# Performance work log

Hardware: AMD Instinct MI355X
Metric: run time of the kernel (lower is better)

## Reference

```python
import jax, jax.numpy as jnp
import numpy as np

N_QUBITS = 7
N_LAYERS = 4
DIM = 2 ** N_QUBITS  # 128
# PennyLane StronglyEntanglingLayers default ranges: (l % (n_wires-1)) + 1
RANGES = [(l % (N_QUBITS - 1)) + 1 for l in range(N_LAYERS)]  # [1,2,3,4]
BATCH = 262144


def rot_matrix(phi, theta, omega):
    """PennyLane Rot(phi, theta, omega) = RZ(omega) RY(theta) RZ(phi)."""
    c = jnp.cos(theta / 2)
    s = jnp.sin(theta / 2)
    a = jnp.exp(-0.5j * (phi + omega)) * c
    b = -jnp.exp(0.5j * (phi - omega)) * s
    cc = jnp.exp(-0.5j * (phi - omega)) * s
    d = jnp.exp(0.5j * (phi + omega)) * c
    return jnp.stack([jnp.stack([a, b]), jnp.stack([cc, d])])  # (2,2) complex64


def apply_1q(psi, U, wire):
    # psi: (batch, 2,2,2,2,2,2,2); apply 2x2 U on qubit axis 1+wire
    psi = jnp.moveaxis(psi, 1 + wire, -1)
    psi = psi @ U.T
    return jnp.moveaxis(psi, -1, 1 + wire)


def apply_cnot(psi, ctrl, tgt):
    psi = jnp.moveaxis(psi, (1 + ctrl, 1 + tgt), (-2, -1))
    # flip target amplitude pair where control == 1
    psi = jnp.concatenate([psi[..., 0:1, :], psi[..., 1:2, ::-1]], axis=-2)
    return jnp.moveaxis(psi, (-2, -1), (1 + ctrl, 1 + tgt))


def setup_inputs() -> dict:
    key = jax.random.key(0)
    k1, k2 = jax.random.split(key)
    x = jax.random.normal(k1, (BATCH, DIM), dtype=jnp.float32)
    weights = jax.random.normal(k2, (N_LAYERS, N_QUBITS, 3), dtype=jnp.float32)
    return {"x": x, "weights": weights}


def reference(x, weights):
    # AmplitudeEmbedding with normalize=True
    norm = jnp.linalg.norm(x, axis=-1, keepdims=True)
    psi = (x / norm).astype(jnp.complex64)
    psi = psi.reshape((-1,) + (2,) * N_QUBITS)

    # StronglyEntanglingLayers
    for l in range(N_LAYERS):
        for w in range(N_QUBITS):
            U = rot_matrix(weights[l, w, 0], weights[l, w, 1], weights[l, w, 2])
            psi = apply_1q(psi, U, w)
        r = RANGES[l]
        for w in range(N_QUBITS):
            psi = apply_cnot(psi, w, (w + r) % N_QUBITS)

    # expval(Z0 @ Z6): sign = (-1)^(b0 + b6)
    probs = (jnp.abs(psi) ** 2).reshape(-1, 2, DIM // 4, 2)  # (batch, q0, mid, q6)
    z = jnp.array([1.0, -1.0], dtype=jnp.float32)
    return jnp.einsum('a,namb,b->n', z, probs, z)
```

## Files before the change

kernel.cpp:

```cpp
#include <hip/hip_runtime.h>


#define N_QUBITS 7
#define DIM 128
#define N_LAYERS 4
#define BATCH 262144
#define GRID 512
#define ROWS 32
#define ITERS (BATCH / (GRID * ROWS))
#define DEPTH 4

typedef short short8 __attribute__((ext_vector_type(8)));
typedef float f32x4 __attribute__((ext_vector_type(4)));
typedef unsigned int u32;
typedef __attribute__((address_space(1))) const u32 g_u32;
typedef __attribute__((address_space(3))) u32 l_u32;

__device__ __forceinline__ unsigned short f2bf(float f) {
  unsigned u = __builtin_bit_cast(unsigned, f);
  u += 0x7fffu + ((u >> 16) & 1u);
  return (unsigned short)(u >> 16);
}

__device__ __forceinline__ unsigned pk2(float x, float y) {
  unsigned ux = __builtin_bit_cast(unsigned, x) + 0x8000u;
  unsigned uy = __builtin_bit_cast(unsigned, y) + 0x8000u;
  return __builtin_amdgcn_perm(uy, ux, 0x07060302u);
}

__device__ __forceinline__ short8 pack_bf16(float4 lo, float4 hi) {
  uint4 d;
  d.x = pk2(lo.x, lo.y);
  d.y = pk2(lo.z, lo.w);
  d.z = pk2(hi.x, hi.y);
  d.w = pk2(hi.z, hi.w);
  return __builtin_bit_cast(short8, d);
}

__global__ void sim_columns(const float* __restrict__ W,
                            float* __restrict__ Ur, float* __restrict__ Ui) {
  __shared__ float sr[DIM], si[DIM];
  const int c = blockIdx.x;
  const int t = threadIdx.x;

  sr[t] = (t == c) ? 1.f : 0.f;        si[t] = 0.f;
  sr[t + 64] = (t + 64 == c) ? 1.f : 0.f;  si[t + 64] = 0.f;
  __syncthreads();

  for (int l = 0; l < N_LAYERS; ++l) {
    for (int w = 0; w < N_QUBITS; ++w) {
      const float phi = W[(l * 7 + w) * 3 + 0];
      const float th  = W[(l * 7 + w) * 3 + 1];
      const float om  = W[(l * 7 + w) * 3 + 2];
      const float ch = __cosf(0.5f * th), sh = __sinf(0.5f * th);
      const float ap = 0.5f * (phi + om), am = 0.5f * (phi - om);
      const float cap = __cosf(ap), sap = __sinf(ap);
      const float cam = __cosf(am), sam = __sinf(am);
      const float ar =  cap * ch, ai = -sap * ch;
      const float br = -cam * sh, bi = -sam * sh;
      const float cr =  cam * sh, ci = -sam * sh;
      const float dr =  cap * ch, di =  sap * ch;

      const int m = 1 << (6 - w);
      const int i0 = ((t & ~(m - 1)) << 1) | (t & (m - 1));
      const int i1 = i0 | m;
      const float x0r = sr[i0], x0i = si[i0];
      const float x1r = sr[i1], x1i = si[i1];
      __syncthreads();
      sr[i0] = ar * x0r - ai * x0i + br * x1r - bi * x1i;
      si[i0] = ar * x0i + ai * x0r + br * x1i + bi * x1r;
      sr[i1] = cr * x0r - ci * x0i + dr * x1r - di * x1i;
      si[i1] = cr * x0i + ci * x0r + dr * x1i + di * x1r;
      __syncthreads();
    }
    const int r = (l % (N_QUBITS - 1)) + 1;
    for (int w = 0; w < N_QUBITS; ++w) {
      const int ctrl = w, tgt = (w + r) % N_QUBITS;
      const int cmask = 1 << (6 - ctrl), tmask = 1 << (6 - tgt);
      const int i0 = ((t & ~(tmask - 1)) << 1) | (t & (tmask - 1));
      const int i1 = i0 | tmask;
      const float a0r = sr[i0], a0i = si[i0];
      const float a1r = sr[i1], a1i = si[i1];
      __syncthreads();
      if (i0 & cmask) {
        sr[i0] = a1r; si[i0] = a1i;
        sr[i1] = a0r; si[i1] = a0i;
      }
      __syncthreads();
    }
  }
  Ur[(size_t)t * DIM + c]        = sr[t];
  Ui[(size_t)t * DIM + c]        = si[t];
  Ur[(size_t)(t + 64) * DIM + c] = sr[t + 64];
  Ui[(size_t)(t + 64) * DIM + c] = si[t + 64];
}

__global__ void build_A(const float* __restrict__ Ur, const float* __restrict__ Ui,
                        unsigned short* __restrict__ Ab) {
  const int i = blockIdx.x;
  const int j = threadIdx.x;
  float s = 0.f;
#pragma unroll 8
  for (int k = 0; k < DIM; ++k) {
    const float zk = (((k >> 6) ^ k) & 1) ? -1.f : 1.f;
    s += zk * (Ur[k * DIM + i] * Ur[k * DIM + j] + Ui[k * DIM + i] * Ui[k * DIM + j]);
  }
  Ab[i * DIM + j] = f2bf(s);
}

__device__ __forceinline__ void stage_half(const float* __restrict__ X, float* XsBuf,
                                           int tile, int wave, int lane) {
#pragma unroll
  for (int j = 0; j < 8; ++j) {
    const int s = 512 * wave + 64 * j + lane;
    const int row = s >> 5;
    const int c = (s & 31) ^ (row & 7);
    const float* gp = X + (size_t)tile * (ROWS * DIM) + row * DIM + c * 4;
    __builtin_amdgcn_global_load_lds((g_u32*)gp, (l_u32*)(XsBuf + s * 4), 16, 0, 0);
  }
}

__global__ __launch_bounds__(128, 1) void vqa_main(const float* __restrict__ X,
                                                   const unsigned short* __restrict__ Ab,
                                                   float* __restrict__ out) {
  __shared__ float Xs[DEPTH * ROWS * DIM];

  const int tid = threadIdx.x;
  const int lane = tid & 63;
  const int wave = tid >> 6;
  const int n16 = lane & 15;
  const int g = lane >> 4;
  const int R = 16 * wave + n16;
  const int rx = R & 7;

  short8 a_frag[4][8];
#pragma unroll
  for (int kt = 0; kt < 4; ++kt)
#pragma unroll
    for (int t = 0; t < 8; ++t)
      a_frag[kt][t] = *reinterpret_cast<const short8*>(
          Ab + (16 * t + n16) * DIM + 32 * kt + 8 * g);

#pragma unroll
  for (int p = 0; p < DEPTH - 1; ++p)
    stage_half(X, Xs + p * (ROWS * DIM), blockIdx.x + p * GRID, wave, lane);

#pragma unroll 1
  for (int it = 0; it < ITERS; ++it) {
    const int cur = it & (DEPTH - 1);

    if (it + DEPTH - 1 < ITERS)
      stage_half(X, Xs + ((it + DEPTH - 1) & (DEPTH - 1)) * (ROWS * DIM),
                 blockIdx.x + (it + DEPTH - 1) * GRID, wave, lane);

    const int rem = ITERS - 1 - it;
    if (rem >= DEPTH - 1)  asm volatile("s_waitcnt vmcnt(24)" ::: "memory");
    else if (rem == 2)     asm volatile("s_waitcnt vmcnt(16)" ::: "memory");
    else if (rem == 1)     asm volatile("s_waitcnt vmcnt(8)"  ::: "memory");
    else                   asm volatile("s_waitcnt vmcnt(0)"  ::: "memory");

    const int rb = cur * (ROWS * 32) + R * 32;

    short8 bfrag[4];
#pragma unroll
    for (int kt = 0; kt < 4; ++kt) {
      const int c0 = 8 * kt + 2 * g;
      const float4 lo = *reinterpret_cast<const float4*>(Xs + (rb + (c0 ^ rx)) * 4);
      const float4 hi = *reinterpret_cast<const float4*>(Xs + (rb + ((c0 + 1) ^ rx)) * 4);
      bfrag[kt] = pack_bf16(lo, hi);
    }

    f32x4 acc[8];
#pragma unroll
    for (int t = 0; t < 8; ++t) acc[t] = (f32x4){0.f, 0.f, 0.f, 0.f};
#pragma unroll
    for (int kt = 0; kt < 4; ++kt) {
#pragma unroll
      for (int t = 0; t < 8; ++t)
        acc[t] = __builtin_amdgcn_mfma_f32_16x16x32_bf16(a_frag[kt][t], bfrag[kt],
                                                         acc[t], 0, 0, 0);
    }

    float dot = 0.f, nrm = 0.f;
#pragma unroll
    for (int t = 0; t < 8; ++t) {
      const float4 xe = *reinterpret_cast<const float4*>(Xs + (rb + ((4 * t + g) ^ rx)) * 4);
      dot += xe.x * acc[t][0] + xe.y * acc[t][1] + xe.z * acc[t][2] + xe.w * acc[t][3];
      nrm += xe.x * xe.x + xe.y * xe.y + xe.z * xe.z + xe.w * xe.w;
    }
    dot += __shfl_xor(dot, 16, 64);
    dot += __shfl_xor(dot, 32, 64);
    nrm += __shfl_xor(nrm, 16, 64);
    nrm += __shfl_xor(nrm, 32, 64);
    if (g == 0) out[(blockIdx.x + it * GRID) * ROWS + R] = dot / nrm;
  }
}

extern "C" void kernel_launch(void* const* d_in, const int* in_sizes, int n_in,
                              void* d_out, int out_size, void* d_ws, size_t ws_size,
                              hipStream_t stream) {
  const float* X = (const float*)d_in[0];
  const float* W = (const float*)d_in[1];
  float* out = (float*)d_out;

  float* Ur = (float*)d_ws;
  float* Ui = Ur + DIM * DIM;
  unsigned short* Ab = (unsigned short*)(Ui + DIM * DIM);

  sim_columns<<<DIM, 64, 0, stream>>>(W, Ur, Ui);
  build_A<<<DIM, DIM, 0, stream>>>(Ur, Ui, Ab);
  vqa_main<<<GRID, 128, 0, stream>>>(X, Ab, out);
}
```

Measured before the change: 208.4 us.

## Fuse circuit simulation, A-matrix build and main GEMV into one persistent kernel

Merges the three launches into a single kernel that uses software grid barriers. The first 128 blocks simulate the unitary columns with wave shuffles in registers instead of LDS plus syncthreads, then build the bf16 observable matrix. All 512 blocks wait on a second barrier before the main streaming loop. The X prefetch is issued before the setup phase so the loads overlap it. This removes launch gaps and the serialized small-kernel latency, but it adds a memset, depends on every block being co-resident for the spin barriers, and the barrier spin costs some time of its own.

```diff
diff --git a/kernel.cpp b/kernel.cpp
--- a/kernel.cpp
+++ b/kernel.cpp
@@ -37,75 +37,16 @@
   return __builtin_bit_cast(short8, d);
 }
 
-__global__ void sim_columns(const float* __restrict__ W,
-                            float* __restrict__ Ur, float* __restrict__ Ui) {
-  __shared__ float sr[DIM], si[DIM];
-  const int c = blockIdx.x;
-  const int t = threadIdx.x;
-
-  sr[t] = (t == c) ? 1.f : 0.f;        si[t] = 0.f;
-  sr[t + 64] = (t + 64 == c) ? 1.f : 0.f;  si[t + 64] = 0.f;
+__device__ __forceinline__ void grid_bar(unsigned* bar, unsigned target) {
+  __threadfence();
   __syncthreads();
-
-  for (int l = 0; l < N_LAYERS; ++l) {
-    for (int w = 0; w < N_QUBITS; ++w) {
-      const float phi = W[(l * 7 + w) * 3 + 0];
-      const float th  = W[(l * 7 + w) * 3 + 1];
-      const float om  = W[(l * 7 + w) * 3 + 2];
-      const float ch = __cosf(0.5f * th), sh = __sinf(0.5f * th);
-      const float ap = 0.5f * (phi + om), am = 0.5f * (phi - om);
-      const float cap = __cosf(ap), sap = __sinf(ap);
-      const float cam = __cosf(am), sam = __sinf(am);
-      const float ar =  cap * ch, ai = -sap * ch;
-      const float br = -cam * sh, bi = -sam * sh;
-      const float cr =  cam * sh, ci = -sam * sh;
-      const float dr =  cap * ch, di =  sap * ch;
-
-      const int m = 1 << (6 - w);
-      const int i0 = ((t & ~(m - 1)) << 1) | (t & (m - 1));
-      const int i1 = i0 | m;
-      const float x0r = sr[i0], x0i = si[i0];
-      const float x1r = sr[i1], x1i = si[i1];
-      __syncthreads();
-      sr[i0] = ar * x0r - ai * x0i + br * x1r - bi * x1i;
-      si[i0] = ar * x0i + ai * x0r + br * x1i + bi * x1r;
-      sr[i1] = cr * x0r - ci * x0i + dr * x1r - di * x1i;
-      si[i1] = cr * x0i + ci * x0r + dr * x1i + di * x1r;
-      __syncthreads();
-    }
-    const int r = (l % (N_QUBITS - 1)) + 1;
-    for (int w = 0; w < N_QUBITS; ++w) {
-      const int ctrl = w, tgt = (w + r) % N_QUBITS;
-      const int cmask = 1 << (6 - ctrl), tmask = 1 << (6 - tgt);
-      const int i0 = ((t & ~(tmask - 1)) << 1) | (t & (tmask - 1));
-      const int i1 = i0 | tmask;
-      const float a0r = sr[i0], a0i = si[i0];
-      const float a1r = sr[i1], a1i = si[i1];
-      __syncthreads();
-      if (i0 & cmask) {
-        sr[i0] = a1r; si[i0] = a1i;
-        sr[i1] = a0r; si[i1] = a0i;
-      }
-      __syncthreads();
-    }
-  }
-  Ur[(size_t)t * DIM + c]        = sr[t];
-  Ui[(size_t)t * DIM + c]        = si[t];
-  Ur[(size_t)(t + 64) * DIM + c] = sr[t + 64];
-  Ui[(size_t)(t + 64) * DIM + c] = si[t + 64];
-}
-
-__global__ void build_A(const float* __restrict__ Ur, const float* __restrict__ Ui,
-                        unsigned short* __restrict__ Ab) {
-  const int i = blockIdx.x;
-  const int j = threadIdx.x;
-  float s = 0.f;
-#pragma unroll 8
-  for (int k = 0; k < DIM; ++k) {
-    const float zk = (((k >> 6) ^ k) & 1) ? -1.f : 1.f;
-    s += zk * (Ur[k * DIM + i] * Ur[k * DIM + j] + Ui[k * DIM + i] * Ui[k * DIM + j]);
-  }
-  Ab[i * DIM + j] = f2bf(s);
+  if (threadIdx.x == 0) {
+    __hip_atomic_fetch_add(bar, 1u, __ATOMIC_ACQ_REL, __HIP_MEMORY_SCOPE_AGENT);
+    while (__hip_atomic_load(bar, __ATOMIC_ACQUIRE, __HIP_MEMORY_SCOPE_AGENT) < target)
+      __builtin_amdgcn_s_sleep(8);
+    __threadfence();
+  }
+  __syncthreads();
 }
 
 __device__ __forceinline__ void stage_half(const float* __restrict__ X, float* XsBuf,
@@ -120,14 +61,111 @@
   }
 }
 
-__global__ __launch_bounds__(128, 1) void vqa_main(const float* __restrict__ X,
-                                                   const unsigned short* __restrict__ Ab,
-                                                   float* __restrict__ out) {
+__global__ __launch_bounds__(128, 1) void vqa_fused(const float* __restrict__ X,
+                                                    const float* __restrict__ W,
+                                                    float* __restrict__ Ur,
+                                                    float* __restrict__ Ui,
+                                                    unsigned short* __restrict__ Ab,
+                                                    unsigned* __restrict__ bars,
+                                                    float* __restrict__ out) {
   __shared__ float Xs[DEPTH * ROWS * DIM];
 
   const int tid = threadIdx.x;
   const int lane = tid & 63;
   const int wave = tid >> 6;
+
+#pragma unroll
+  for (int p = 0; p < DEPTH - 1; ++p)
+    stage_half(X, Xs + p * (ROWS * DIM), blockIdx.x + p * GRID, wave, lane);
+
+  if (blockIdx.x < DIM) {
+    if (wave == 0) {
+      const int c = blockIdx.x;
+      float r0r = (lane == c) ? 1.f : 0.f, r0i = 0.f;
+      float r1r = (lane + 64 == c) ? 1.f : 0.f, r1i = 0.f;
+
+      for (int l = 0; l < N_LAYERS; ++l) {
+        for (int w = 0; w < N_QUBITS; ++w) {
+          const float phi = W[(l * 7 + w) * 3 + 0];
+          const float th  = W[(l * 7 + w) * 3 + 1];
+          const float om  = W[(l * 7 + w) * 3 + 2];
+          const float ch = __cosf(0.5f * th), sh = __sinf(0.5f * th);
+          const float ap = 0.5f * (phi + om), am = 0.5f * (phi - om);
+          const float cap = __cosf(ap), sap = __sinf(ap);
+          const float cam = __cosf(am), sam = __sinf(am);
+          const float ar =  cap * ch, ai = -sap * ch;
+          const float br = -cam * sh, bi = -sam * sh;
+          const float cr =  cam * sh, ci = -sam * sh;
+          const float dr =  cap * ch, di =  sap * ch;
+
+          const int m = 1 << (6 - w);
+          if (m == 64) {
+            const float n0r = ar * r0r - ai * r0i + br * r1r - bi * r1i;
+            const float n0i = ar * r0i + ai * r0r + br * r1i + bi * r1r;
+            const float n1r = cr * r0r - ci * r0i + dr * r1r - di * r1i;
+            const float n1i = cr * r0i + ci * r0r + dr * r1i + di * r1r;
+            r0r = n0r; r0i = n0i; r1r = n1r; r1i = n1i;
+          } else {
+            const bool hi = (lane & m) != 0;
+            const float u_r = hi ? dr : ar, u_i = hi ? di : ai;
+            const float v_r = hi ? cr : br, v_i = hi ? ci : bi;
+            float pr, pi, nr, ni;
+            pr = __shfl_xor(r0r, m, 64); pi = __shfl_xor(r0i, m, 64);
+            nr = u_r * r0r - u_i * r0i + v_r * pr - v_i * pi;
+            ni = u_r * r0i + u_i * r0r + v_r * pi + v_i * pr;
+            r0r = nr; r0i = ni;
+            pr = __shfl_xor(r1r, m, 64); pi = __shfl_xor(r1i, m, 64);
+            nr = u_r * r1r - u_i * r1i + v_r * pr - v_i * pi;
+            ni = u_r * r1i + u_i * r1r + v_r * pi + v_i * pr;
+            r1r = nr; r1i = ni;
+          }
+        }
+        const int rr = (l % (N_QUBITS - 1)) + 1;
+        for (int w = 0; w < N_QUBITS; ++w) {
+          const int tgt = (w + rr) % N_QUBITS;
+          const int mc = 1 << (6 - w), mt = 1 << (6 - tgt);
+          if (mt == 64) {
+            const bool s = (lane & mc) != 0;
+            const float t0r = s ? r1r : r0r, t1r = s ? r0r : r1r;
+            const float t0i = s ? r1i : r0i, t1i = s ? r0i : r1i;
+            r0r = t0r; r1r = t1r; r0i = t0i; r1i = t1i;
+          } else if (mc == 64) {
+            r1r = __shfl_xor(r1r, mt, 64);
+            r1i = __shfl_xor(r1i, mt, 64);
+          } else {
+            const bool s = (lane & mc) != 0;
+            float t;
+            t = __shfl_xor(r0r, mt, 64); r0r = s ? t : r0r;
+            t = __shfl_xor(r0i, mt, 64); r0i = s ? t : r0i;
+            t = __shfl_xor(r1r, mt, 64); r1r = s ? t : r1r;
+            t = __shfl_xor(r1i, mt, 64); r1i = s ? t : r1i;
+          }
+        }
+      }
+      const int c2 = blockIdx.x;
+      Ur[(size_t)lane * DIM + c2]        = r0r;
+      Ui[(size_t)lane * DIM + c2]        = r0i;
+      Ur[(size_t)(lane + 64) * DIM + c2] = r1r;
+      Ui[(size_t)(lane + 64) * DIM + c2] = r1i;
+    }
+    grid_bar(&bars[0], DIM);
+
+    {
+      const int i = blockIdx.x;
+      const int j = tid;
+      float s = 0.f;
+#pragma unroll 8
+      for (int k = 0; k < DIM; ++k) {
+        const float zk = (((k >> 6) ^ k) & 1) ? -1.f : 1.f;
+        s += zk * (Ur[k * DIM + i] * Ur[k * DIM + j] + Ui[k * DIM + i] * Ui[k * DIM + j]);
+      }
+      Ab[i * DIM + j] = f2bf(s);
+    }
+  }
+
+  grid_bar(&bars[1], GRID);
+  asm volatile("s_waitcnt vmcnt(0)" ::: "memory");
+
   const int n16 = lane & 15;
   const int g = lane >> 4;
   const int R = 16 * wave + n16;
@@ -140,10 +178,6 @@
     for (int t = 0; t < 8; ++t)
       a_frag[kt][t] = *reinterpret_cast<const short8*>(
           Ab + (16 * t + n16) * DIM + 32 * kt + 8 * g);
-
-#pragma unroll
-  for (int p = 0; p < DEPTH - 1; ++p)
-    stage_half(X, Xs + p * (ROWS * DIM), blockIdx.x + p * GRID, wave, lane);
 
 #pragma unroll 1
   for (int it = 0; it < ITERS; ++it) {
@@ -206,8 +240,9 @@
   float* Ur = (float*)d_ws;
   float* Ui = Ur + DIM * DIM;
   unsigned short* Ab = (unsigned short*)(Ui + DIM * DIM);
-
-  sim_columns<<<DIM, 64, 0, stream>>>(W, Ur, Ui);
-  build_A<<<DIM, DIM, 0, stream>>>(Ur, Ui, Ab);
-  vqa_main<<<GRID, 128, 0, stream>>>(X, Ab, out);
-}
+  unsigned* bars = (unsigned*)(Ab + DIM * DIM);
+
+  hipMemsetAsync(bars, 0, 2 * sizeof(unsigned), stream);
+
+  vqa_fused<<<GRID, 128, 0, stream>>>(X, W, Ur, Ui, Ab, bars, out);
+}
```

After: 331.1 us. 58.9% more time.

## Replace LDS async staging with direct register loads and double the grid

Applied to the files above, without the earlier changes.

Removes the global_load_lds multi-buffer staging through shared memory and instead loads each row's operands straight from global memory into registers. Only the first half of each B fragment is prefetched one iteration ahead, while the second half and the epilogue reads are issued within the iteration (the epilogue reads are likely to hit cache). The grid is doubled and launch bounds allow two blocks per CU to recover latency hiding through occupancy. In exchange it loses the deep explicit prefetch pipeline, adds redundant global/cache reads of X, and shortens the per-block loop.

```diff
diff --git a/kernel.cpp b/kernel.cpp
--- a/kernel.cpp
+++ b/kernel.cpp
@@ -5,16 +5,12 @@
 #define DIM 128
 #define N_LAYERS 4
 #define BATCH 262144
-#define GRID 512
+#define GRID 1024
 #define ROWS 32
 #define ITERS (BATCH / (GRID * ROWS))
-#define DEPTH 4
 
 typedef short short8 __attribute__((ext_vector_type(8)));
 typedef float f32x4 __attribute__((ext_vector_type(4)));
-typedef unsigned int u32;
-typedef __attribute__((address_space(1))) const u32 g_u32;
-typedef __attribute__((address_space(3))) u32 l_u32;
 
 __device__ __forceinline__ unsigned short f2bf(float f) {
   unsigned u = __builtin_bit_cast(unsigned, f);
@@ -108,30 +104,23 @@
   Ab[i * DIM + j] = f2bf(s);
 }
 
-__device__ __forceinline__ void stage_half(const float* __restrict__ X, float* XsBuf,
-                                           int tile, int wave, int lane) {
-#pragma unroll
-  for (int j = 0; j < 8; ++j) {
-    const int s = 512 * wave + 64 * j + lane;
-    const int row = s >> 5;
-    const int c = (s & 31) ^ (row & 7);
-    const float* gp = X + (size_t)tile * (ROWS * DIM) + row * DIM + c * 4;
-    __builtin_amdgcn_global_load_lds((g_u32*)gp, (l_u32*)(XsBuf + s * 4), 16, 0, 0);
-  }
-}
-
-__global__ __launch_bounds__(128, 1) void vqa_main(const float* __restrict__ X,
+__global__ __launch_bounds__(128, 2) void vqa_main(const float* __restrict__ X,
                                                    const unsigned short* __restrict__ Ab,
                                                    float* __restrict__ out) {
-  __shared__ float Xs[DEPTH * ROWS * DIM];
-
   const int tid = threadIdx.x;
   const int lane = tid & 63;
   const int wave = tid >> 6;
   const int n16 = lane & 15;
   const int g = lane >> 4;
   const int R = 16 * wave + n16;
-  const int rx = R & 7;
+
+  const size_t step = (size_t)GRID * ROWS * DIM;
+  const float* p = X + (size_t)blockIdx.x * (ROWS * DIM) + R * DIM;
+
+  float4 lo[4];
+#pragma unroll
+  for (int kt = 0; kt < 4; ++kt)
+    lo[kt] = *reinterpret_cast<const float4*>(p + 32 * kt + 8 * g);
 
   short8 a_frag[4][8];
 #pragma unroll
@@ -141,34 +130,25 @@
       a_frag[kt][t] = *reinterpret_cast<const short8*>(
           Ab + (16 * t + n16) * DIM + 32 * kt + 8 * g);
 
-#pragma unroll
-  for (int p = 0; p < DEPTH - 1; ++p)
-    stage_half(X, Xs + p * (ROWS * DIM), blockIdx.x + p * GRID, wave, lane);
-
 #pragma unroll 1
   for (int it = 0; it < ITERS; ++it) {
-    const int cur = it & (DEPTH - 1);
+    float4 hi[4];
+#pragma unroll
+    for (int kt = 0; kt < 4; ++kt)
+      hi[kt] = *reinterpret_cast<const float4*>(p + 32 * kt + 8 * g + 4);
 
-    if (it + DEPTH - 1 < ITERS)
-      stage_half(X, Xs + ((it + DEPTH - 1) & (DEPTH - 1)) * (ROWS * DIM),
-                 blockIdx.x + (it + DEPTH - 1) * GRID, wave, lane);
-
-    const int rem = ITERS - 1 - it;
-    if (rem >= DEPTH - 1)  asm volatile("s_waitcnt vmcnt(24)" ::: "memory");
-    else if (rem == 2)     asm volatile("s_waitcnt vmcnt(16)" ::: "memory");
-    else if (rem == 1)     asm volatile("s_waitcnt vmcnt(8)"  ::: "memory");
-    else                   asm volatile("s_waitcnt vmcnt(0)"  ::: "memory");
-
-    const int rb = cur * (ROWS * 32) + R * 32;
+    float4 nlo[4];
+    const bool more = (it + 1 < ITERS);
+    if (more) {
+#pragma unroll
+      for (int kt = 0; kt < 4; ++kt)
+        nlo[kt] = *reinterpret_cast<const float4*>(p + step + 32 * kt + 8 * g);
+    }
 
     short8 bfrag[4];
 #pragma unroll
-    for (int kt = 0; kt < 4; ++kt) {
-      const int c0 = 8 * kt + 2 * g;
-      const float4 lo = *reinterpret_cast<const float4*>(Xs + (rb + (c0 ^ rx)) * 4);
-      const float4 hi = *reinterpret_cast<const float4*>(Xs + (rb + ((c0 + 1) ^ rx)) * 4);
-      bfrag[kt] = pack_bf16(lo, hi);
-    }
+    for (int kt = 0; kt < 4; ++kt)
+      bfrag[kt] = pack_bf16(lo[kt], hi[kt]);
 
     f32x4 acc[8];
 #pragma unroll
@@ -184,7 +164,7 @@
     float dot = 0.f, nrm = 0.f;
 #pragma unroll
     for (int t = 0; t < 8; ++t) {
-      const float4 xe = *reinterpret_cast<const float4*>(Xs + (rb + ((4 * t + g) ^ rx)) * 4);
+      const float4 xe = *reinterpret_cast<const float4*>(p + 16 * t + 4 * g);
       dot += xe.x * acc[t][0] + xe.y * acc[t][1] + xe.z * acc[t][2] + xe.w * acc[t][3];
       nrm += xe.x * xe.x + xe.y * xe.y + xe.z * xe.z + xe.w * xe.w;
     }
@@ -193,6 +173,12 @@
     nrm += __shfl_xor(nrm, 16, 64);
     nrm += __shfl_xor(nrm, 32, 64);
     if (g == 0) out[(blockIdx.x + it * GRID) * ROWS + R] = dot / nrm;
+
+    if (more) {
+#pragma unroll
+      for (int kt = 0; kt < 4; ++kt) lo[kt] = nlo[kt];
+    }
+    p += step;
   }
 }
 
```

Result: slower. 216.1 us (+3.7%).
